# Optimization experiments

Measured on AMD Instinct MI355X. Metric: run time of the kernel, lower is better.

Reference implementation:

```python
import jax, jax.numpy as jnp
import numpy as np
import math

MIN_NORM = 1e-15
PROJ_EPS = 4e-3  # float32 boundary eps used by HGCN PoincareBall
C = 1.0          # curvature


def _artanh(x):
    return jnp.arctanh(jnp.clip(x, -1.0 + 1e-7, 1.0 - 1e-7))


def proj(x, c):
    norm = jnp.maximum(jnp.linalg.norm(x, axis=-1, keepdims=True), MIN_NORM)
    maxnorm = (1.0 - PROJ_EPS) / jnp.sqrt(c)
    return jnp.where(norm > maxnorm, x / norm * maxnorm, x)


def lambda_x(x, c):
    x2 = jnp.sum(x * x, axis=-1, keepdims=True)
    return 2.0 / jnp.maximum(1.0 - c * x2, MIN_NORM)


def mobius_add(x, y, c):
    x2 = jnp.sum(x * x, axis=-1, keepdims=True)
    y2 = jnp.sum(y * y, axis=-1, keepdims=True)
    xy = jnp.sum(x * y, axis=-1, keepdims=True)
    num = (1.0 + 2.0 * c * xy + c * y2) * x + (1.0 - c * x2) * y
    denom = 1.0 + 2.0 * c * xy + (c ** 2) * x2 * y2
    return num / jnp.maximum(denom, MIN_NORM)


def logmap0(p, c):
    sqrt_c = jnp.sqrt(c)
    p_norm = jnp.maximum(jnp.linalg.norm(p, axis=-1, keepdims=True), MIN_NORM)
    return _artanh(sqrt_c * p_norm) * p / (p_norm * sqrt_c)


def logmap(p1, p2, c):
    # tangent vector at p1 pointing to p2
    sub = mobius_add(-p1, p2, c)
    sub_norm = jnp.maximum(jnp.linalg.norm(sub, axis=-1, keepdims=True), MIN_NORM)
    lam = lambda_x(p1, c)
    sqrt_c = jnp.sqrt(c)
    return 2.0 / (sqrt_c * lam) * _artanh(sqrt_c * sub_norm) * sub / sub_norm


def expmap(u, p, c):
    # exp map of tangent u at base point p
    sqrt_c = jnp.sqrt(c)
    u_norm = jnp.maximum(jnp.linalg.norm(u, axis=-1, keepdims=True), MIN_NORM)
    second = jnp.tanh(sqrt_c / 2.0 * lambda_x(p, c) * u_norm) * u / (sqrt_c * u_norm)
    return mobius_add(p, second, c)


def setup_inputs() -> dict:
    key = jax.random.key(0)
    k1, k2, k3 = jax.random.split(key, 3)
    N, D = 768, 128
    x = jax.random.normal(k1, (N, D), jnp.float32) * 0.1
    x = proj(x, C)  # valid points on the Poincare ball
    adj = (jax.random.uniform(k2, (N, N), jnp.float32) < 0.04).astype(jnp.float32)
    att_w = jax.random.normal(k3, (2 * D, 1), jnp.float32) * (1.0 / math.sqrt(2 * D))
    att_b = jnp.zeros((1,), jnp.float32)
    return {"x": x, "adj": adj, "att_w": att_w, "att_b": att_b}


def reference(x, adj, att_w, att_b):
    c = C
    D = x.shape[-1]
    x_tangent = logmap0(x, c)                               # [N, D]
    # pairwise logmap: tangent at x_i pointing to x_j -> [N, N, D]
    x_local_tangent = logmap(x[:, None, :], x[None, :, :], c)
    # DenseAtt: sigmoid(Linear([xt_i ; xt_j])) * adj, factorized to avoid [N,N,2D]
    s_left = x_tangent @ att_w[:D, 0]                        # [N]
    s_right = x_tangent @ att_w[D:, 0]                       # [N]
    adj_att = jax.nn.sigmoid(s_left[:, None] + s_right[None, :] + att_b[0]) * adj
    support_t = jnp.einsum('ij,ijd->id', adj_att, x_local_tangent)  # [N, D]
    output = proj(expmap(support_t, x, c), c)
    return output
```

## Files before the change

kernel.cpp:

```cpp
#include <hip/hip_runtime.h>
#include <math.h>

#define NN 768
#define DD 128
#define XC 64
#define MAXN 128

__global__ __launch_bounds__(256) void hypagg_fused(
        const float* __restrict__ x, const float* __restrict__ adj,
        const float* __restrict__ att_w, const float* __restrict__ att_b,
        float* __restrict__ out) {
    __shared__ float  xcache[XC][DD];
    __shared__ int    list[MAXN];
    __shared__ float  aval[MAXN];
    __shared__ float  bco[MAXN];
    __shared__ double upart[DD];
    __shared__ int    counter;
    __shared__ double s_x2i, s_sLi;
    __shared__ double cpart[4];
    __shared__ double epart[2][3];

    const int i = blockIdx.x, t = threadIdx.x;
    const int wid = t >> 6, lane = t & 63;
    const int g = t >> 4, gl = t & 15;

    float4 adjv = make_float4(0.f, 0.f, 0.f, 0.f);
    if (t >= 64) adjv = ((const float4*)(adj + (size_t)i * NN))[t - 64];
    float xv = 0.0f;
    if (t < DD) xv = x[(size_t)i * DD + t];
    const float4 xa = ((const float4*)(x + (size_t)i * DD))[gl];
    const float4 xb = ((const float4*)(x + (size_t)i * DD))[16 + gl];
    const float4 wa = ((const float4*)(att_w + DD))[gl];
    const float4 wb = ((const float4*)(att_w + DD))[16 + gl];
    const double b0 = (double)att_b[0];

    if (t == 0) counter = 0;
    __syncthreads();

    if (t >= 64) {
        int m = (adjv.x != 0.0f) + (adjv.y != 0.0f) + (adjv.z != 0.0f) + (adjv.w != 0.0f);
        if (m) {
            int base = atomicAdd(&counter, m);
            int j = 4 * (t - 64);
            if (adjv.x != 0.0f && base < MAXN) { list[base] = j;     aval[base] = adjv.x; ++base; }
            if (adjv.y != 0.0f && base < MAXN) { list[base] = j + 1; aval[base] = adjv.y; ++base; }
            if (adjv.z != 0.0f && base < MAXN) { list[base] = j + 2; aval[base] = adjv.z; ++base; }
            if (adjv.w != 0.0f && base < MAXN) { list[base] = j + 3; aval[base] = adjv.w; ++base; }
        }
    } else {
        const float2 xv2 = ((const float2*)(x + (size_t)i * DD))[lane];
        const float2 wl2 = ((const float2*)att_w)[lane];
        double dx2 = (double)xv2.x * xv2.x + (double)xv2.y * xv2.y;
        double dl  = (double)xv2.x * wl2.x + (double)xv2.y * wl2.y;
        #pragma unroll
        for (int o = 32; o > 0; o >>= 1) {
            dx2 += __shfl_down(dx2, o, 64);
            dl  += __shfl_down(dl,  o, 64);
        }
        if (lane == 0) {
            double r  = sqrt(dx2);
            double g0 = atanh(fmin(r, 1.0 - 1e-7)) / fmax(r, 1e-15);
            s_x2i = dx2;
            s_sLi = g0 * dl;
        }
    }
    __syncthreads();
    const int n = (counter < MAXN) ? counter : MAXN;

    double asum = 0.0;
    {
        const double x2i = s_x2i, sLi = s_sLi;
        const double beta = 1.0 - x2i;
        const double factor = fmax(beta, 1e-15);
        for (int k = g; k < n; k += 16) {
            const float4* xj4 = (const float4*)(x + (size_t)list[k] * DD);
            float4 a = xj4[gl];
            float4 b = xj4[16 + gl];
            if (k < XC) {
                ((float4*)xcache[k])[gl]      = a;
                ((float4*)xcache[k])[16 + gl] = b;
            }
            double dd = (double)xa.x * a.x + (double)xa.y * a.y
                      + (double)xa.z * a.z + (double)xa.w * a.w
                      + (double)xb.x * b.x + (double)xb.y * b.y
                      + (double)xb.z * b.z + (double)xb.w * b.w;
            double yy = (double)a.x * a.x + (double)a.y * a.y
                      + (double)a.z * a.z + (double)a.w * a.w
                      + (double)b.x * b.x + (double)b.y * b.y
                      + (double)b.z * b.z + (double)b.w * b.w;
            double ww = (double)wa.x * a.x + (double)wa.y * a.y
                      + (double)wa.z * a.z + (double)wa.w * a.w
                      + (double)wb.x * b.x + (double)wb.y * b.y
                      + (double)wb.z * b.z + (double)wb.w * b.w;
            #pragma unroll
            for (int o = 8; o > 0; o >>= 1) {
                dd += __shfl_down(dd, o, 16);
                yy += __shfl_down(yy, o, 16);
                ww += __shfl_down(ww, o, 16);
            }
            if (gl == 0) {
                double dot = dd;
                double y2  = yy;
                double ry  = sqrt(y2);
                double g0j = atanh(fmin(ry, 1.0 - 1e-7)) / fmax(ry, 1e-15);
                double z   = sLi + g0j * ww + b0;
                double w   = (double)aval[k] / (1.0 + exp(-z));
                double alpha  = 1.0 - 2.0 * dot + y2;
                double denomc = fmax(1.0 - 2.0 * dot + x2i * y2, 1e-15);
                double sn2 = (alpha * alpha * x2i - 2.0 * alpha * beta * dot + beta * beta * y2)
                             / (denomc * denomc);
                double sn  = fmax(sqrt(fmax(sn2, 0.0)), 1e-15);
                double gg  = atanh(fmin(sn, 1.0 - 1e-7)) / sn;
                double common = w * factor * gg / denomc;
                asum -= common * alpha;
                bco[k] = (float)(common * beta);
            }
        }
    }
    #pragma unroll
    for (int o = 32; o > 0; o >>= 1) asum += __shfl_down(asum, o, 64);
    if (lane == 0) cpart[wid] = asum;
    __syncthreads();

    double u = 0.0;
    {
        const int d = t & (DD - 1);
        const int h = t >> 7;
        double p = 0.0;
        const int nc = (n < XC) ? n : XC;
        for (int k = h; k < nc; k += 2) p += (double)bco[k] * (double)xcache[k][d];
        for (int k = XC + h; k < n; k += 2) p += (double)bco[k] * (double)x[(size_t)list[k] * DD + d];
        if (h == 1) upart[d] = p;
        __syncthreads();
        if (t < DD) {
            const double rowA = cpart[0] + cpart[1] + cpart[2] + cpart[3];
            u = rowA * (double)xv + p + upart[d];
            double p_un2 = u * u;
            double p_xu  = (double)xv * u;
            #pragma unroll
            for (int o = 32; o > 0; o >>= 1) {
                p_un2 += __shfl_down(p_un2, o, 64);
                p_xu  += __shfl_down(p_xu,  o, 64);
            }
            if (lane == 0) { epart[wid][0] = p_un2; epart[wid][1] = p_xu; }
        }
    }
    __syncthreads();

    double ov = 0.0;
    if (t < DD) {
        double un2 = epart[0][0] + epart[1][0];
        double xu  = epart[0][1] + epart[1][1];
        double x2i = s_x2i;
        double lamfac = fmax(1.0 - x2i, 1e-15);
        double un = fmax(sqrt(un2), 1e-15);
        double th = tanh(un / lamfac);
        double s  = th / un;
        double y2 = s * s * un2;
        double xy = s * xu;
        double c1 = 1.0 + 2.0 * xy + y2;
        double c2 = 1.0 - x2i;
        double den = fmax(1.0 + 2.0 * xy + x2i * y2, 1e-15);
        ov = (c1 * (double)xv + c2 * s * u) / den;
        double p_on2 = ov * ov;
        #pragma unroll
        for (int o = 32; o > 0; o >>= 1) p_on2 += __shfl_down(p_on2, o, 64);
        if (lane == 0) epart[wid][2] = p_on2;
    }
    __syncthreads();

    if (t < DD) {
        double on2 = epart[0][2] + epart[1][2];
        double on  = fmax(sqrt(on2), 1e-15);
        const double maxn = 1.0 - 4e-3;
        double scale = (on > maxn) ? (maxn / on) : 1.0;
        out[i * DD + t] = (float)(ov * scale);
    }
}

extern "C" void kernel_launch(void* const* d_in, const int* in_sizes, int n_in,
                              void* d_out, int out_size, void* d_ws, size_t ws_size,
                              hipStream_t stream) {
    const float* x     = (const float*)d_in[0];
    const float* adj   = (const float*)d_in[1];
    const float* att_w = (const float*)d_in[2];
    const float* att_b = (const float*)d_in[3];
    float* out = (float*)d_out;
    (void)d_ws; (void)ws_size;

    hypagg_fused<<<NN, 256, 0, stream>>>(x, adj, att_w, att_b, out);
}
```

Baseline: 74.69 us.

## Rewrite aggregation as one wavefront per row with ballot compaction

Each row is now handled by a single 64-lane wavefront instead of a 256-thread block. The neighbor list is built with ballot/popcount prefix compaction rather than shared-memory atomics, and cross-wave shared partials are replaced by xor shuffles. The per-neighbor scalar math now runs lane-parallel after the dot products are staged in LDS. The goal is to cut block-level synchronisation and shrink shared memory so more rows fit per CU, at the cost of fewer threads per row and dropping the x_j LDS cache in favour of re-reading x_j from global/L2. MAXN is lowered to 96, which silently truncates any row with more neighbors.

```diff
diff --git a/kernel.cpp b/kernel.cpp
--- a/kernel.cpp
+++ b/kernel.cpp
@@ -3,179 +3,162 @@
 
 #define NN 768
 #define DD 128
-#define XC 64
-#define MAXN 128
+#define MAXN 96
 
-__global__ __launch_bounds__(256) void hypagg_fused(
+__global__ __launch_bounds__(64) void hypagg_wave(
         const float* __restrict__ x, const float* __restrict__ adj,
         const float* __restrict__ att_w, const float* __restrict__ att_b,
         float* __restrict__ out) {
-    __shared__ float  xcache[XC][DD];
     __shared__ int    list[MAXN];
     __shared__ float  aval[MAXN];
+    __shared__ double dots[MAXN];
+    __shared__ double y2s[MAXN];
+    __shared__ double wrs[MAXN];
     __shared__ float  bco[MAXN];
-    __shared__ double upart[DD];
-    __shared__ int    counter;
-    __shared__ double s_x2i, s_sLi;
-    __shared__ double cpart[4];
-    __shared__ double epart[2][3];
 
-    const int i = blockIdx.x, t = threadIdx.x;
-    const int wid = t >> 6, lane = t & 63;
-    const int g = t >> 4, gl = t & 15;
+    const int i    = blockIdx.x;
+    const int lane = threadIdx.x;
+    const int gl   = lane & 15;
+    const int g    = lane >> 4;
 
-    float4 adjv = make_float4(0.f, 0.f, 0.f, 0.f);
-    if (t >= 64) adjv = ((const float4*)(adj + (size_t)i * NN))[t - 64];
-    float xv = 0.0f;
-    if (t < DD) xv = x[(size_t)i * DD + t];
-    const float4 xa = ((const float4*)(x + (size_t)i * DD))[gl];
-    const float4 xb = ((const float4*)(x + (size_t)i * DD))[16 + gl];
-    const float4 wa = ((const float4*)(att_w + DD))[gl];
-    const float4 wb = ((const float4*)(att_w + DD))[16 + gl];
-    const double b0 = (double)att_b[0];
+    const float4 adjv0 = ((const float4*)(adj + (size_t)i * NN))[lane];
+    const float4 adjv1 = ((const float4*)(adj + (size_t)i * NN))[lane + 64];
+    const float4 adjv2 = ((const float4*)(adj + (size_t)i * NN))[lane + 128];
+    const float2 xv2 = ((const float2*)(x + (size_t)i * DD))[lane];
+    const float2 wl2 = ((const float2*)att_w)[lane];
+    const float4 xa  = ((const float4*)(x + (size_t)i * DD))[gl];
+    const float4 xb  = ((const float4*)(x + (size_t)i * DD))[16 + gl];
+    const float4 wa  = ((const float4*)(att_w + DD))[gl];
+    const float4 wb  = ((const float4*)(att_w + DD))[16 + gl];
+    const double b0  = (double)att_b[0];
 
-    if (t == 0) counter = 0;
+    double dx2 = (double)xv2.x * xv2.x + (double)xv2.y * xv2.y;
+    double dl  = (double)xv2.x * wl2.x + (double)xv2.y * wl2.y;
+    #pragma unroll
+    for (int o = 32; o > 0; o >>= 1) {
+        dx2 += __shfl_xor(dx2, o, 64);
+        dl  += __shfl_xor(dl,  o, 64);
+    }
+    const double x2i = dx2;
+    {
+    }
+    double r_  = sqrt(dx2);
+    double g0i = atanh(fmin(r_, 1.0 - 1e-7)) / fmax(r_, 1e-15);
+    const double sLi = g0i * dl;
+
+    int n = 0;
+    {
+        const unsigned long long below = (lane == 0) ? 0ull : (~0ull >> (64 - lane));
+        const float vals[12] = {adjv0.x, adjv0.y, adjv0.z, adjv0.w,
+                                adjv1.x, adjv1.y, adjv1.z, adjv1.w,
+                                adjv2.x, adjv2.y, adjv2.z, adjv2.w};
+        #pragma unroll
+        for (int rnd = 0; rnd < 12; ++rnd) {
+            float v = vals[rnd];
+            unsigned long long m = __ballot(v != 0.0f);
+            if (v != 0.0f) {
+                int pos = n + __popcll(m & below);
+                if (pos < MAXN) {
+                    list[pos] = 4 * ((rnd >> 2) * 64 + lane) + (rnd & 3);
+                    aval[pos] = v;
+                }
+            }
+            n += __popcll(m);
+        }
+        if (n > MAXN) n = MAXN;
+    }
     __syncthreads();
 
-    if (t >= 64) {
-        int m = (adjv.x != 0.0f) + (adjv.y != 0.0f) + (adjv.z != 0.0f) + (adjv.w != 0.0f);
-        if (m) {
-            int base = atomicAdd(&counter, m);
-            int j = 4 * (t - 64);
-            if (adjv.x != 0.0f && base < MAXN) { list[base] = j;     aval[base] = adjv.x; ++base; }
-            if (adjv.y != 0.0f && base < MAXN) { list[base] = j + 1; aval[base] = adjv.y; ++base; }
-            if (adjv.z != 0.0f && base < MAXN) { list[base] = j + 2; aval[base] = adjv.z; ++base; }
-            if (adjv.w != 0.0f && base < MAXN) { list[base] = j + 3; aval[base] = adjv.w; ++base; }
+    for (int k = g; k < n; k += 4) {
+        const float4* xj4 = (const float4*)(x + (size_t)list[k] * DD);
+        float4 a = xj4[gl];
+        float4 b = xj4[16 + gl];
+        double dd = (double)xa.x * a.x + (double)xa.y * a.y
+                  + (double)xa.z * a.z + (double)xa.w * a.w
+                  + (double)xb.x * b.x + (double)xb.y * b.y
+                  + (double)xb.z * b.z + (double)xb.w * b.w;
+        double yy = (double)a.x * a.x + (double)a.y * a.y
+                  + (double)a.z * a.z + (double)a.w * a.w
+                  + (double)b.x * b.x + (double)b.y * b.y
+                  + (double)b.z * b.z + (double)b.w * b.w;
+        double ww = (double)wa.x * a.x + (double)wa.y * a.y
+                  + (double)wa.z * a.z + (double)wa.w * a.w
+                  + (double)wb.x * b.x + (double)wb.y * b.y
+                  + (double)wb.z * b.z + (double)wb.w * b.w;
+        #pragma unroll
+        for (int o = 8; o > 0; o >>= 1) {
+            dd += __shfl_down(dd, o, 16);
+            yy += __shfl_down(yy, o, 16);
+            ww += __shfl_down(ww, o, 16);
         }
-    } else {
-        const float2 xv2 = ((const float2*)(x + (size_t)i * DD))[lane];
-        const float2 wl2 = ((const float2*)att_w)[lane];
-        double dx2 = (double)xv2.x * xv2.x + (double)xv2.y * xv2.y;
-        double dl  = (double)xv2.x * wl2.x + (double)xv2.y * wl2.y;
-        #pragma unroll
-        for (int o = 32; o > 0; o >>= 1) {
-            dx2 += __shfl_down(dx2, o, 64);
-            dl  += __shfl_down(dl,  o, 64);
-        }
-        if (lane == 0) {
-            double r  = sqrt(dx2);
-            double g0 = atanh(fmin(r, 1.0 - 1e-7)) / fmax(r, 1e-15);
-            s_x2i = dx2;
-            s_sLi = g0 * dl;
-        }
+        if (gl == 0) { dots[k] = dd; y2s[k] = yy; wrs[k] = ww; }
     }
     __syncthreads();
-    const int n = (counter < MAXN) ? counter : MAXN;
 
     double asum = 0.0;
     {
-        const double x2i = s_x2i, sLi = s_sLi;
-        const double beta = 1.0 - x2i;
+        const double beta   = 1.0 - x2i;
         const double factor = fmax(beta, 1e-15);
-        for (int k = g; k < n; k += 16) {
-            const float4* xj4 = (const float4*)(x + (size_t)list[k] * DD);
-            float4 a = xj4[gl];
-            float4 b = xj4[16 + gl];
-            if (k < XC) {
-                ((float4*)xcache[k])[gl]      = a;
-                ((float4*)xcache[k])[16 + gl] = b;
-            }
-            double dd = (double)xa.x * a.x + (double)xa.y * a.y
-                      + (double)xa.z * a.z + (double)xa.w * a.w
-                      + (double)xb.x * b.x + (double)xb.y * b.y
-                      + (double)xb.z * b.z + (double)xb.w * b.w;
-            double yy = (double)a.x * a.x + (double)a.y * a.y
-                      + (double)a.z * a.z + (double)a.w * a.w
-                      + (double)b.x * b.x + (double)b.y * b.y
-                      + (double)b.z * b.z + (double)b.w * b.w;
-            double ww = (double)wa.x * a.x + (double)wa.y * a.y
-                      + (double)wa.z * a.z + (double)wa.w * a.w
-                      + (double)wb.x * b.x + (double)wb.y * b.y
-                      + (double)wb.z * b.z + (double)wb.w * b.w;
-            #pragma unroll
-            for (int o = 8; o > 0; o >>= 1) {
-                dd += __shfl_down(dd, o, 16);
-                yy += __shfl_down(yy, o, 16);
-                ww += __shfl_down(ww, o, 16);
-            }
-            if (gl == 0) {
-                double dot = dd;
-                double y2  = yy;
-                double ry  = sqrt(y2);
-                double g0j = atanh(fmin(ry, 1.0 - 1e-7)) / fmax(ry, 1e-15);
-                double z   = sLi + g0j * ww + b0;
-                double w   = (double)aval[k] / (1.0 + exp(-z));
-                double alpha  = 1.0 - 2.0 * dot + y2;
-                double denomc = fmax(1.0 - 2.0 * dot + x2i * y2, 1e-15);
-                double sn2 = (alpha * alpha * x2i - 2.0 * alpha * beta * dot + beta * beta * y2)
-                             / (denomc * denomc);
-                double sn  = fmax(sqrt(fmax(sn2, 0.0)), 1e-15);
-                double gg  = atanh(fmin(sn, 1.0 - 1e-7)) / sn;
-                double common = w * factor * gg / denomc;
-                asum -= common * alpha;
-                bco[k] = (float)(common * beta);
-            }
+        for (int k = lane; k < n; k += 64) {
+            double dot = dots[k];
+            double y2  = y2s[k];
+            double ww  = wrs[k];
+            double ry  = sqrt(y2);
+            double g0j = atanh(fmin(ry, 1.0 - 1e-7)) / fmax(ry, 1e-15);
+            double z   = sLi + g0j * ww + b0;
+            double w   = (double)aval[k] / (1.0 + exp(-z));
+            double alpha  = 1.0 - 2.0 * dot + y2;
+            double denomc = fmax(1.0 - 2.0 * dot + x2i * y2, 1e-15);
+            double sn2 = (alpha * alpha * x2i - 2.0 * alpha * beta * dot + beta * beta * y2)
+                         / (denomc * denomc);
+            double sn  = fmax(sqrt(fmax(sn2, 0.0)), 1e-15);
+            double gg  = atanh(fmin(sn, 1.0 - 1e-7)) / sn;
+            double common = w * factor * gg / denomc;
+            asum -= common * alpha;
+            bco[k] = (float)(common * beta);
         }
     }
     #pragma unroll
-    for (int o = 32; o > 0; o >>= 1) asum += __shfl_down(asum, o, 64);
-    if (lane == 0) cpart[wid] = asum;
+    for (int o = 32; o > 0; o >>= 1) asum += __shfl_xor(asum, o, 64);
     __syncthreads();
 
-    double u = 0.0;
-    {
-        const int d = t & (DD - 1);
-        const int h = t >> 7;
-        double p = 0.0;
-        const int nc = (n < XC) ? n : XC;
-        for (int k = h; k < nc; k += 2) p += (double)bco[k] * (double)xcache[k][d];
-        for (int k = XC + h; k < n; k += 2) p += (double)bco[k] * (double)x[(size_t)list[k] * DD + d];
-        if (h == 1) upart[d] = p;
-        __syncthreads();
-        if (t < DD) {
-            const double rowA = cpart[0] + cpart[1] + cpart[2] + cpart[3];
-            u = rowA * (double)xv + p + upart[d];
-            double p_un2 = u * u;
-            double p_xu  = (double)xv * u;
-            #pragma unroll
-            for (int o = 32; o > 0; o >>= 1) {
-                p_un2 += __shfl_down(p_un2, o, 64);
-                p_xu  += __shfl_down(p_xu,  o, 64);
-            }
-            if (lane == 0) { epart[wid][0] = p_un2; epart[wid][1] = p_xu; }
-        }
+    double ux = asum * (double)xv2.x;
+    double uy = asum * (double)xv2.y;
+    #pragma unroll 4
+    for (int k = 0; k < n; ++k) {
+        double b = (double)bco[k];
+        float2 xj = ((const float2*)(x + (size_t)list[k] * DD))[lane];
+        ux += b * (double)xj.x;
+        uy += b * (double)xj.y;
     }
-    __syncthreads();
 
-    double ov = 0.0;
-    if (t < DD) {
-        double un2 = epart[0][0] + epart[1][0];
-        double xu  = epart[0][1] + epart[1][1];
-        double x2i = s_x2i;
-        double lamfac = fmax(1.0 - x2i, 1e-15);
-        double un = fmax(sqrt(un2), 1e-15);
-        double th = tanh(un / lamfac);
-        double s  = th / un;
-        double y2 = s * s * un2;
-        double xy = s * xu;
-        double c1 = 1.0 + 2.0 * xy + y2;
-        double c2 = 1.0 - x2i;
-        double den = fmax(1.0 + 2.0 * xy + x2i * y2, 1e-15);
-        ov = (c1 * (double)xv + c2 * s * u) / den;
-        double p_on2 = ov * ov;
-        #pragma unroll
-        for (int o = 32; o > 0; o >>= 1) p_on2 += __shfl_down(p_on2, o, 64);
-        if (lane == 0) epart[wid][2] = p_on2;
+    double p_un2 = ux * ux + uy * uy;
+    double p_xu  = (double)xv2.x * ux + (double)xv2.y * uy;
+    #pragma unroll
+    for (int o = 32; o > 0; o >>= 1) {
+        p_un2 += __shfl_xor(p_un2, o, 64);
+        p_xu  += __shfl_xor(p_xu,  o, 64);
     }
-    __syncthreads();
+    double lamfac = fmax(1.0 - x2i, 1e-15);
+    double un = fmax(sqrt(p_un2), 1e-15);
+    double th = tanh(un / lamfac);
+    double s  = th / un;
+    double y2 = s * s * p_un2;
+    double xy = s * p_xu;
+    double c1 = 1.0 + 2.0 * xy + y2;
+    double c2 = 1.0 - x2i;
+    double den = fmax(1.0 + 2.0 * xy + x2i * y2, 1e-15);
+    double ovx = (c1 * (double)xv2.x + c2 * s * ux) / den;
+    double ovy = (c1 * (double)xv2.y + c2 * s * uy) / den;
 
-    if (t < DD) {
-        double on2 = epart[0][2] + epart[1][2];
-        double on  = fmax(sqrt(on2), 1e-15);
-        const double maxn = 1.0 - 4e-3;
-        double scale = (on > maxn) ? (maxn / on) : 1.0;
-        out[i * DD + t] = (float)(ov * scale);
-    }
+    double p_on2 = ovx * ovx + ovy * ovy;
+    #pragma unroll
+    for (int o = 32; o > 0; o >>= 1) p_on2 += __shfl_xor(p_on2, o, 64);
+    double on = fmax(sqrt(p_on2), 1e-15);
+    const double maxn_ = 1.0 - 4e-3;
+    double scale = (on > maxn_) ? (maxn_ / on) : 1.0;
+    ((float2*)(out + (size_t)i * DD))[lane] =
+        make_float2((float)(ovx * scale), (float)(ovy * scale));
 }
 
 extern "C" void kernel_launch(void* const* d_in, const int* in_sizes, int n_in,
@@ -188,5 +171,5 @@
     float* out = (float*)d_out;
     (void)d_ws; (void)ws_size;
 
-    hypagg_fused<<<NN, 256, 0, stream>>>(x, adj, att_w, att_b, out);
+    hypagg_wave<<<NN, 64, 0, stream>>>(x, adj, att_w, att_b, out);
 }
```

Measured after the change: 72.07 us. 3.5% less time.
